# Kernel tuning notes

Measured on AMD Instinct MI355X. Metric: run time of the kernel, lower is better.

The kernel has to match this reference:

```python
import jax, jax.numpy as jnp
import numpy as np

B, L, H, V, P = 256, 16, 256, 5000, 4
NPG, DEG, STEPS, OUT = 150, 4, 4, 2000
N, E = B * NPG, B * NPG * DEG


def _seg_softmax(x, seg, num):
    # sparse softmax over variable-size groups (rows of the sparse matrix)
    m = jax.ops.segment_max(x, seg, num_segments=num)
    e = jnp.exp(x - m[seg])
    s = jax.ops.segment_sum(e, seg, num_segments=num)
    return e / s[seg]


def setup_inputs():
    key = jax.random.key(0)
    ks = jax.random.split(key, 24)
    questions = jax.random.normal(ks[0], (B, L, H), jnp.float32)
    lengths = jax.random.randint(ks[1], (B,), L // 2, L + 1)
    node_attrs = jax.random.normal(ks[2], (N, P - 1, H), jnp.float32)
    edge_attrs = jax.random.normal(ks[3], (E, H), jnp.float32)
    node_graph = jnp.repeat(jnp.arange(B), NPG)
    edge_graph = jnp.repeat(jnp.arange(B), NPG * DEG)
    off = jnp.repeat(jnp.arange(B) * NPG, NPG * DEG)
    edge_src = jax.random.randint(ks[4], (E,), 0, NPG) + off
    edge_dst = jax.random.randint(ks[5], (E,), 0, NPG) + off
    s = float(1.0 / np.sqrt(H))
    u = lambda k, shape: jax.random.uniform(k, shape, jnp.float32, -s, s)
    vocab = jax.random.normal(ks[6], (V, H), jnp.float32) * 0.1
    default_embed = jax.random.uniform(ks[7], (H,), jnp.float32)
    W_norm = jnp.eye(H, dtype=jnp.float32)
    lstm_Wih, lstm_Whh = u(ks[8], (4 * H, H)), u(ks[9], (4 * H, H))
    lstm_bih, lstm_bhh = u(ks[10], (4 * H,)), u(ks[11], (4 * H,))
    rnn_Wih, rnn_Whh = u(ks[12], (H, H)), u(ks[13], (H, H))
    rnn_bih, rnn_bhh = u(ks[14], (H,)), u(ks[15], (H,))
    prop_embeds = jax.random.normal(ks[16], (P, H), jnp.float32) * 0.1
    Ws_property = jax.random.uniform(ks[17], (P, H, H), jnp.float32) * s
    W_state = jax.random.uniform(ks[18], (H,), jnp.float32) * s
    W_relation = jax.random.uniform(ks[19], (H,), jnp.float32) * s
    lin_W, lin_b = u(ks[20], (OUT, 2 * H)), u(ks[21], (OUT,))
    return dict(questions=questions, node_attrs=node_attrs, edge_attrs=edge_attrs,
                vocab=vocab, default_embed=default_embed, W_norm=W_norm,
                lstm_Wih=lstm_Wih, lstm_Whh=lstm_Whh, lstm_bih=lstm_bih, lstm_bhh=lstm_bhh,
                rnn_Wih=rnn_Wih, rnn_Whh=rnn_Whh, rnn_bih=rnn_bih, rnn_bhh=rnn_bhh,
                prop_embeds=prop_embeds, Ws_property=Ws_property,
                W_state=W_state, W_relation=W_relation, lin_W=lin_W, lin_b=lin_b,
                lengths=lengths, node_graph=node_graph, edge_graph=edge_graph,
                edge_src=edge_src, edge_dst=edge_dst)


def reference(questions, node_attrs, edge_attrs, vocab, default_embed, W_norm,
              lstm_Wih, lstm_Whh, lstm_bih, lstm_bhh,
              rnn_Wih, rnn_Whh, rnn_bih, rnn_bhh,
              prop_embeds, Ws_property, W_state, W_relation, lin_W, lin_b,
              lengths, node_graph, edge_graph, edge_src, edge_dst):
    # ---- NormalizeWordsModel (tagger) ----
    words = questions.reshape(B * L, H)
    C = jnp.concatenate([vocab, default_embed[None]], axis=0)  # [V+1, H]
    Pm = jax.nn.softmax((words @ W_norm) @ C.T, axis=1)        # [B*L, V+1]
    Vtag = Pm[:, -1:] * words + Pm[:, :-1] @ vocab             # [B*L, H]
    Vpad = Vtag.reshape(B, L, H)

    # ---- LSTM encoder: final hidden at last valid step (packed-sequence semantics) ----
    valid = jnp.arange(L)[:, None] < lengths[None, :]  # [L, B]

    def lstm_step(carry, inp):
        h, c = carry
        x, v = inp
        g = x @ lstm_Wih.T + lstm_bih + h @ lstm_Whh.T + lstm_bhh
        i, f, gc, o = jnp.split(g, 4, axis=-1)  # torch gate order i,f,g,o
        c_new = jax.nn.sigmoid(f) * c + jax.nn.sigmoid(i) * jnp.tanh(gc)
        h_new = jax.nn.sigmoid(o) * jnp.tanh(c_new)
        vm = v[:, None]
        return (jnp.where(vm, h_new, h), jnp.where(vm, c_new, c)), None

    z = jnp.zeros((B, H), questions.dtype)
    (Q, _), _ = jax.lax.scan(lstm_step, (z, z), (Vpad.transpose(1, 0, 2), valid))

    # ---- InstructionsDecoder: relu RNNCell fed the same Q each step ----
    def dec_step(hx, _):
        hx = jax.nn.relu(Q @ rnn_Wih.T + rnn_bih + hx @ rnn_Whh.T + rnn_bhh)
        return hx, hx

    _, Hins = jax.lax.scan(dec_step, z, None, length=STEPS)
    Hins = Hins.transpose(1, 0, 2)  # [B, STEPS, H]

    # ---- attention over (masked) tagged words ----
    att = jnp.einsum('bnh,blh->bnl', Hins, Vpad)
    mask = jnp.arange(L)[None, None, :] < lengths[:, None, None]
    att = jnp.where(mask, att, -jnp.inf)
    R = jax.nn.softmax(att, axis=-1) @ Vpad  # instructions [B, STEPS, H]

    # ---- NSMCell recurrence ----
    nodes_per_graph = jax.ops.segment_sum(jnp.ones(N, questions.dtype), node_graph, num_segments=B)
    dist = (1.0 / nodes_per_graph)[node_graph]  # [N]
    prop_sim = None
    for step in range(STEPS):
        instr = R[:, step]  # [B, H]
        prop_sim = jax.nn.softmax(instr @ prop_embeds.T, axis=1)  # [B, P]
        transformed = jnp.einsum('phk,npk->nph', Ws_property[:-1], node_attrs)  # [N, P-1, H]
        node_scores = jax.nn.elu(jnp.sum(
            prop_sim[node_graph, :-1, None] * instr[node_graph, None, :] * transformed, axis=1))  # [N, H]
        edge_scores = jax.nn.elu(instr[edge_graph] * (edge_attrs @ Ws_property[-1].T))  # [E, H]
        p_state = _seg_softmax(node_scores @ W_state, node_graph, B)  # [N]
        agg = jax.ops.segment_sum(dist[edge_src, None] * edge_scores, edge_dst, num_segments=N)  # [N, H]
        p_rel = _seg_softmax(agg @ W_relation, node_graph, B)  # [N]
        r = prop_sim[node_graph, -1]
        dist = r * p_rel + (1.0 - r) * p_state

    # ---- readout ----
    node_feat = jnp.sum(prop_sim[node_graph, :-1, None] * node_attrs, axis=1)  # [N, H]
    aggregated = jax.ops.segment_sum(dist[:, None] * node_feat, node_graph, num_segments=B)  # [B, H]
    return jnp.concatenate([Q, aggregated], axis=1) @ lin_W.T + lin_b
```

## Files before the change

### kernel.cpp

```cpp
#include <hip/hip_runtime.h>
#include <hip/hip_bf16.h>
#include <math.h>

#define BB 256
#define LL 16
#define HH 256
#define VV 5000
#define NPG 150
#define DEG 4
#define NSTEPS 4
#define OUTD 2000
#define NN (BB*NPG)
#define EE (BB*NPG*DEG)
#define BL (BB*LL)
#define VPAD 5120
#define KPAD 5024

__device__ __forceinline__ float wred_sum(float v){
  #pragma unroll
  for(int o=32;o;o>>=1) v += __shfl_down(v,o,64);
  return v;
}
__device__ __forceinline__ float wred_max(float v){
  #pragma unroll
  for(int o=32;o;o>>=1) v = fmaxf(v,__shfl_down(v,o,64));
  return v;
}
__device__ __forceinline__ float block_sum256(float v, float* sh){
  v = wred_sum(v);
  __syncthreads();
  if((threadIdx.x&63)==0) sh[threadIdx.x>>6]=v;
  __syncthreads();
  return sh[0]+sh[1]+sh[2]+sh[3];
}
__device__ __forceinline__ float block_max256(float v, float* sh){
  v = wred_max(v);
  __syncthreads();
  if((threadIdx.x&63)==0) sh[threadIdx.x>>6]=v;
  __syncthreads();
  return fmaxf(fmaxf(sh[0],sh[1]),fmaxf(sh[2],sh[3]));
}
__device__ __forceinline__ float eluf(float x){ return x>0.f ? x : expm1f(x); }
__device__ __forceinline__ float sigf(float x){ return 1.f/(1.f+expf(-x)); }
__device__ __forceinline__ float fsig(float x){
  return __builtin_amdgcn_rcpf(1.f + __expf(-x));
}
__device__ __forceinline__ float ftanh(float x){
  return 1.f - 2.f*__builtin_amdgcn_rcpf(1.f + __expf(2.f*x));
}
__device__ __forceinline__ float b2f(unsigned short s){
  union{float f; unsigned int u;} x; x.u = ((unsigned int)s)<<16; return x.f;
}
__device__ __forceinline__ unsigned short f2bf_bits(float x){
  union { __hip_bfloat16 h; unsigned short s; } u; u.h = __float2bfloat16(x); return u.s;
}

__device__ __forceinline__ void async16(void* lds, const void* g){
  __builtin_amdgcn_global_load_lds(
      (const __attribute__((address_space(1))) unsigned int*)g,
      (__attribute__((address_space(3))) unsigned int*)lds, 16, 0, 0);
}

typedef __attribute__((ext_vector_type(8))) short short8;
typedef __attribute__((ext_vector_type(4))) float f32x4;

__device__ __forceinline__ short8 pack8(float4 a, float4 b){
  short8 r;
  r[0]=(short)f2bf_bits(a.x); r[1]=(short)f2bf_bits(a.y);
  r[2]=(short)f2bf_bits(a.z); r[3]=(short)f2bf_bits(a.w);
  r[4]=(short)f2bf_bits(b.x); r[5]=(short)f2bf_bits(b.y);
  r[6]=(short)f2bf_bits(b.z); r[7]=(short)f2bf_bits(b.w);
  return r;
}

template<int EPI>
__global__ __launch_bounds__(256) void mfma_bt_bf16_k(
    const __hip_bfloat16* __restrict__ A, const __hip_bfloat16* __restrict__ Bt,
    float* __restrict__ Cf, __hip_bfloat16* __restrict__ Cb,
    int lda, int ldb, int ldc, int Nreal,
    int kItersTotal, int kPerSplit, const float* __restrict__ bias,
    const float* __restrict__ rscale)
{
  __shared__ __hip_bfloat16 As[128*32];
  __shared__ __hip_bfloat16 Bs[128*32];
  const int bm = blockIdx.y*128, bn = blockIdx.x*128;
  const int tid = threadIdx.x;
  int k0 = blockIdx.z * kPerSplit;
  int k1 = k0 + kPerSplit; if (k1 > kItersTotal) k1 = kItersTotal;
  const int lane = tid & 63, wave = tid >> 6;
  const int quad = lane >> 4, r16 = lane & 15;
  const int wr = wave >> 1, wc = wave & 1;
  f32x4 acc[4][4] = {};
  const int c0 = tid, c1 = tid + 256;
  const int ar0 = c0 >> 2, ak0 = (c0 & 3)*8;
  const int ar1 = c1 >> 2, ak1 = (c1 & 3)*8;
  const __hip_bfloat16* Ab = A + (size_t)bm*lda;
  const __hip_bfloat16* Bb = Bt + (size_t)bn*ldb;
  for (int kk = k0; kk < k1; ++kk){
    const int kb = kk*32;
    async16(&As[c0*8], Ab + (size_t)ar0*lda + kb + ak0);
    async16(&As[c1*8], Ab + (size_t)ar1*lda + kb + ak1);
    async16(&Bs[c0*8], Bb + (size_t)ar0*ldb + kb + ak0);
    async16(&Bs[c1*8], Bb + (size_t)ar1*ldb + kb + ak1);
    __syncthreads();
    short8 av[4], bv[4];
    #pragma unroll
    for (int i=0;i<4;i++){
      av[i] = *(const short8*)&As[(wr*64 + i*16 + r16)*32 + quad*8];
      bv[i] = *(const short8*)&Bs[(wc*64 + i*16 + r16)*32 + quad*8];
    }
    #pragma unroll
    for (int i=0;i<4;i++)
      #pragma unroll
      for (int j=0;j<4;j++)
        acc[i][j] = __builtin_amdgcn_mfma_f32_16x16x32_bf16(av[i], bv[j], acc[i][j], 0,0,0);
    __syncthreads();
  }
  #pragma unroll
  for (int i=0;i<4;i++){
    int row = bm + wr*64 + i*16 + quad*4;
    #pragma unroll
    for (int j=0;j<4;j++){
      int col = bn + wc*64 + j*16 + r16;
      if (col >= Nreal) continue;
      #pragma unroll
      for (int r=0;r<4;r++){
        float v = acc[i][j][r];
        if (EPI==0){ if (bias) v += bias[col]; Cf[(size_t)(row+r)*ldc + col] = v; }
        else if (EPI==1){ Cb[(size_t)(row+r)*ldc + col] = __float2bfloat16(v); }
        else { if (rscale) v *= rscale[row+r]; atomicAdd(&Cf[(size_t)(row+r)*ldc + col], v); }
      }
    }
  }
}

template<int EPI>
__global__ __launch_bounds__(256) void mfma_bt_f32_k(
    const float* __restrict__ A, const float* __restrict__ Bt,
    float* __restrict__ Cf, __hip_bfloat16* __restrict__ Cb,
    int lda, int ldb, int ldc, int Nreal,
    int kIters, const float* __restrict__ bias)
{
  __shared__ __hip_bfloat16 As[128*32];
  __shared__ __hip_bfloat16 Bs[128*32];
  const int bm = blockIdx.y*128, bn = blockIdx.x*128;
  const int tid = threadIdx.x;
  const int lane = tid & 63, wave = tid >> 6;
  const int quad = lane >> 4, r16 = lane & 15;
  const int wr = wave >> 1, wc = wave & 1;
  f32x4 acc[4][4] = {};
  for (int kk = 0; kk < kIters; ++kk){
    const int kb = kk*32;
    #pragma unroll
    for (int i=0;i<2;i++){
      int c = tid + i*256;
      int row = c >> 2, k0 = (c & 3)*8;
      const float* src = A + (size_t)(bm+row)*lda + kb + k0;
      float4 v0 = *(const float4*)(src);
      float4 v1 = *(const float4*)(src+4);
      *(short8*)&As[row*32 + k0] = pack8(v0, v1);
    }
    #pragma unroll
    for (int i=0;i<2;i++){
      int c = tid + i*256;
      int row = c >> 2, k0 = (c & 3)*8;
      float4 v0 = {0.f,0.f,0.f,0.f}, v1 = {0.f,0.f,0.f,0.f};
      if (bn + row < Nreal){
        const float* src = Bt + (size_t)(bn+row)*ldb + kb + k0;
        v0 = *(const float4*)(src);
        v1 = *(const float4*)(src+4);
      }
      *(short8*)&Bs[row*32 + k0] = pack8(v0, v1);
    }
    __syncthreads();
    short8 av[4], bv[4];
    #pragma unroll
    for (int i=0;i<4;i++){
      av[i] = *(const short8*)&As[(wr*64 + i*16 + r16)*32 + quad*8];
      bv[i] = *(const short8*)&Bs[(wc*64 + i*16 + r16)*32 + quad*8];
    }
    #pragma unroll
    for (int i=0;i<4;i++)
      #pragma unroll
      for (int j=0;j<4;j++)
        acc[i][j] = __builtin_amdgcn_mfma_f32_16x16x32_bf16(av[i], bv[j], acc[i][j], 0,0,0);
    __syncthreads();
  }
  #pragma unroll
  for (int i=0;i<4;i++){
    int row = bm + wr*64 + i*16 + quad*4;
    #pragma unroll
    for (int j=0;j<4;j++){
      int col = bn + wc*64 + j*16 + r16;
      if (col >= Nreal) continue;
      #pragma unroll
      for (int r=0;r<4;r++){
        float v = acc[i][j][r];
        if (EPI==0){ if (bias) v += bias[col]; Cf[(size_t)(row+r)*ldc + col] = v; }
        else { Cb[(size_t)(row+r)*ldc + col] = __float2bfloat16(v); }
      }
    }
  }
}

__global__ __launch_bounds__(256) void gemm_exp_k(
    const __hip_bfloat16* __restrict__ A, const __hip_bfloat16* __restrict__ Bt,
    __hip_bfloat16* __restrict__ Pm, float* __restrict__ row_sum,
    float* __restrict__ e_def)
{
  __shared__ __hip_bfloat16 As[128*32];
  __shared__ __hip_bfloat16 Bs[128*32];
  const int bm = blockIdx.y*128, bn = blockIdx.x*128;
  const int tid = threadIdx.x;
  const int lane = tid & 63, wave = tid >> 6;
  const int quad = lane >> 4, r16 = lane & 15;
  const int wr = wave >> 1, wc = wave & 1;
  f32x4 acc[4][4] = {};
  const int c0 = tid, c1 = tid + 256;
  const int ar0 = c0 >> 2, ak0 = (c0 & 3)*8;
  const int ar1 = c1 >> 2, ak1 = (c1 & 3)*8;
  const __hip_bfloat16* Ab = A + (size_t)bm*HH;
  const __hip_bfloat16* Bb = Bt + (size_t)bn*HH;
  for (int kk = 0; kk < HH/32; ++kk){
    const int kb = kk*32;
    async16(&As[c0*8], Ab + (size_t)ar0*HH + kb + ak0);
    async16(&As[c1*8], Ab + (size_t)ar1*HH + kb + ak1);
    async16(&Bs[c0*8], Bb + (size_t)ar0*HH + kb + ak0);
    async16(&Bs[c1*8], Bb + (size_t)ar1*HH + kb + ak1);
    __syncthreads();
    short8 av[4], bv[4];
    #pragma unroll
    for (int i=0;i<4;i++){
      av[i] = *(const short8*)&As[(wr*64 + i*16 + r16)*32 + quad*8];
      bv[i] = *(const short8*)&Bs[(wc*64 + i*16 + r16)*32 + quad*8];
    }
    #pragma unroll
    for (int i=0;i<4;i++)
      #pragma unroll
      for (int j=0;j<4;j++)
        acc[i][j] = __builtin_amdgcn_mfma_f32_16x16x32_bf16(av[i], bv[j], acc[i][j], 0,0,0);
    __syncthreads();
  }
  #pragma unroll
  for (int i=0;i<4;i++){
    int rowb = bm + wr*64 + i*16 + quad*4;
    float rsum[4] = {0.f,0.f,0.f,0.f};
    #pragma unroll
    for (int j=0;j<4;j++){
      int col = bn + wc*64 + j*16 + r16;
      #pragma unroll
      for (int r=0;r<4;r++){
        float e = (col <= VV) ? expf(acc[i][j][r]) : 0.f;
        rsum[r] += e;
        if (col < KPAD) Pm[(size_t)(rowb+r)*KPAD + col] = __float2bfloat16(col < VV ? e : 0.f);
        if (col == VV) e_def[rowb+r] = e;
      }
    }
    #pragma unroll
    for (int r=0;r<4;r++){
      float s = rsum[r];
      s += __shfl_xor(s, 1, 64);
      s += __shfl_xor(s, 2, 64);
      s += __shfl_xor(s, 4, 64);
      s += __shfl_xor(s, 8, 64);
      if (r16 == 0) atomicAdd(&row_sum[rowb+r], s);
    }
  }
}

__global__ __launch_bounds__(1024, 4) void lstm_persist_k(
    const float* __restrict__ gX, const __hip_bfloat16* __restrict__ Whh_bf,
    const int* __restrict__ lengths,
    float* __restrict__ h_out, __hip_bfloat16* __restrict__ hbf_out)
{
  __shared__ __hip_bfloat16 Wl[512*132];
  __shared__ __hip_bfloat16 hbuf[2][16*264];
  const int bg = blockIdx.x, tid = threadIdx.x;
  const int lane = tid & 63, w = tid >> 6;
  const int quad = lane >> 4, r16 = lane & 15;
  const int hb = w*16;
  for (int idx = tid; idx < 512*16; idx += 1024){
    int row = idx >> 4, c8 = (idx & 15)*8;
    int ww = row >> 6, g = (row >> 4) & 3, rr = row & 15;
    *(short8*)&Wl[row*132 + c8] =
        *(const short8*)&Whh_bf[((size_t)(g*256 + ww*16 + rr))*256 + 128 + c8];
  }
  short8 rW[4][4];
  #pragma unroll
  for (int kc=0; kc<4; kc++)
    #pragma unroll
    for (int g=0; g<4; g++)
      rW[kc][g] = *(const short8*)&Whh_bf[((size_t)(g*256 + hb + r16))*256 + kc*32 + quad*8];
  for (int i = tid; i < 16*264; i += 1024) hbuf[0][i] = __float2bfloat16(0.f);
  int lenr[4];
  #pragma unroll
  for (int r=0;r<4;r++) lenr[r] = lengths[bg*16 + quad*4 + r];
  __syncthreads();
  f32x4 cstate = {0.f,0.f,0.f,0.f};
  f32x4 hstate = {0.f,0.f,0.f,0.f};
  int p = 0;
  const float* gXb = gX + (size_t)bg*16*LL*(4*HH) + hb + r16;
  for (int t=0; t<LL; t++){
    float gxv[4][4];
    #pragma unroll
    for (int r=0;r<4;r++)
      #pragma unroll
      for (int g=0;g<4;g++)
        gxv[r][g] = gXb[((size_t)((quad*4+r)*LL + t))*(4*HH) + g*HH];
    f32x4 acc[4] = {};
    const __hip_bfloat16* hr = hbuf[p];
    #pragma unroll
    for (int kc=0; kc<4; kc++){
      short8 a = *(const short8*)&hr[r16*264 + kc*32 + quad*8];
      #pragma unroll
      for (int g=0; g<4; g++)
        acc[g] = __builtin_amdgcn_mfma_f32_16x16x32_bf16(a, rW[kc][g], acc[g], 0,0,0);
    }
    if (w < 8){
      #pragma unroll
      for (int kc=4; kc<8; kc++){
        short8 a = *(const short8*)&hr[r16*264 + kc*32 + quad*8];
        #pragma unroll
        for (int g=0; g<4; g++){
          short8 b = *(const short8*)&Wl[(w*64 + g*16 + r16)*132 + (kc-4)*32 + quad*8];
          acc[g] = __builtin_amdgcn_mfma_f32_16x16x32_bf16(a, b, acc[g], 0,0,0);
        }
      }
    } else {
      #pragma unroll
      for (int kc=4; kc<8; kc++){
        short8 a = *(const short8*)&hr[r16*264 + kc*32 + quad*8];
        #pragma unroll
        for (int g=0; g<4; g++){
          short8 b = *(const short8*)&Whh_bf[((size_t)(g*256 + hb + r16))*256 + kc*32 + quad*8];
          acc[g] = __builtin_amdgcn_mfma_f32_16x16x32_bf16(a, b, acc[g], 0,0,0);
        }
      }
    }
    #pragma unroll
    for (int r=0;r<4;r++){
      int batch = quad*4 + r;
      float gi = acc[0][r] + gxv[r][0];
      float gf = acc[1][r] + gxv[r][1];
      float gc = acc[2][r] + gxv[r][2];
      float go = acc[3][r] + gxv[r][3];
      float cn = fsig(gf)*cstate[r] + fsig(gi)*ftanh(gc);
      float hn = fsig(go)*ftanh(cn);
      if (t < lenr[r]){ cstate[r] = cn; hstate[r] = hn; }
      hbuf[p^1][batch*264 + hb + r16] = __float2bfloat16(hstate[r]);
    }
    p ^= 1;
    __syncthreads();
  }
  #pragma unroll
  for (int r=0;r<4;r++){
    int batch = quad*4 + r;
    size_t o = (size_t)(bg*16+batch)*HH + hb + r16;
    h_out[o] = hstate[r];
    hbf_out[o] = __float2bfloat16(hstate[r]);
  }
}

__global__ __launch_bounds__(1024, 4) void dec_persist_k(
    const __hip_bfloat16* __restrict__ Qbf, const __hip_bfloat16* __restrict__ Wih_bf,
    const __hip_bfloat16* __restrict__ Whh_bf,
    const float* __restrict__ bih, const float* __restrict__ bhh,
    float* __restrict__ Hins)
{
  __shared__ __hip_bfloat16 Wl[256*264];
  __shared__ __hip_bfloat16 xb[2][16*264];
  const int bg = blockIdx.x, tid = threadIdx.x;
  const int lane = tid & 63, w = tid >> 6;
  const int quad = lane >> 4, r16 = lane & 15;
  const int col = w*16 + r16;
  for (int c = tid; c < 8192; c += 1024){
    int row = c >> 5, ci = (c & 31)*8;
    *(short8*)&Wl[row*264 + ci] = *(const short8*)&Whh_bf[(size_t)row*256 + ci];
  }
  f32x4 qp = {};
  #pragma unroll
  for (int kc=0; kc<8; kc++){
    short8 a = *(const short8*)&Qbf[(size_t)(bg*16 + r16)*HH + kc*32 + quad*8];
    short8 b = *(const short8*)&Wih_bf[(size_t)col*HH + kc*32 + quad*8];
    qp = __builtin_amdgcn_mfma_f32_16x16x32_bf16(a, b, qp, 0,0,0);
  }
  const float bihv = bih[col], bhhv = bhh[col];
  __syncthreads();
  #pragma unroll
  for (int r=0;r<4;r++){
    int batch = quad*4 + r;
    float v = fmaxf(qp[r] + bihv + bhhv, 0.f);
    xb[0][batch*264 + col] = __float2bfloat16(v);
    Hins[(size_t)(bg*16+batch)*(NSTEPS*HH) + 0*HH + col] = v;
  }
  __syncthreads();
  int p = 0;
  for (int s=1; s<NSTEPS; s++){
    f32x4 acc = {};
    #pragma unroll
    for (int kc=0; kc<8; kc++){
      short8 a = *(const short8*)&xb[p][r16*264 + kc*32 + quad*8];
      short8 b = *(const short8*)&Wl[col*264 + kc*32 + quad*8];
      acc = __builtin_amdgcn_mfma_f32_16x16x32_bf16(a, b, acc, 0,0,0);
    }
    #pragma unroll
    for (int r=0;r<4;r++){
      int batch = quad*4 + r;
      float v = fmaxf(qp[r] + bihv + acc[r] + bhhv, 0.f);
      xb[p^1][batch*264 + col] = __float2bfloat16(v);
      Hins[(size_t)(bg*16+batch)*(NSTEPS*HH) + s*HH + col] = v;
    }
    p ^= 1;
    __syncthreads();
  }
}

__global__ void cvt_bf16_k(const float* __restrict__ src, __hip_bfloat16* __restrict__ dst, int n){
  int i = (blockIdx.x*256 + threadIdx.x)*4;
  if (i >= n) return;
  float4 v = *(const float4*)(src + i);
  dst[i]   = __float2bfloat16(v.x);
  dst[i+1] = __float2bfloat16(v.y);
  dst[i+2] = __float2bfloat16(v.z);
  dst[i+3] = __float2bfloat16(v.w);
}

__global__ void tr_cvt_k(const float* __restrict__ src, __hip_bfloat16* __restrict__ dst, int R, int Ccols){
  int idx = blockIdx.x*256 + threadIdx.x;
  if (idx >= R*Ccols) return;
  int r = idx / Ccols, c = idx % Ccols;
  dst[(size_t)c*R + r] = __float2bfloat16(src[idx]);
}

__global__ void build_cb_k(const float* __restrict__ vocab, const float* __restrict__ de,
                           __hip_bfloat16* __restrict__ Cb){
  int idx = blockIdx.x*256 + threadIdx.x;
  if (idx >= VPAD*HH) return;
  int v = idx >> 8, h = idx & 255;
  float x = (v < VV) ? vocab[(size_t)v*HH + h] : (v == VV ? de[h] : 0.f);
  Cb[idx] = __float2bfloat16(x);
}

__global__ void build_vt_k(const float* __restrict__ vocab, __hip_bfloat16* __restrict__ VT){
  int idx = blockIdx.x*256 + threadIdx.x;
  if (idx >= HH*KPAD) return;
  int h = idx / KPAD, v = idx % KPAD;
  VT[idx] = __float2bfloat16(v < VV ? vocab[(size_t)v*HH + h] : 0.f);
}

__global__ void bsum_k(const float* a, const float* b, float* o){
  int i = blockIdx.x*256 + threadIdx.x;
  if (i < 4*HH) o[i] = a[i] + b[i];
}

__global__ void init_k(float* dist, float* s_rel){
  int idx = blockIdx.x*256 + threadIdx.x;
  if (idx < NN){ dist[idx] = 1.f/150.f; s_rel[idx] = 0.f; }
}

__global__ void zero_k(float* p, int n){
  int idx = blockIdx.x*256 + threadIdx.x;
  if (idx < n) p[idx] = 0.f;
}

__global__ void inv_k(float* p, int n){
  int idx = blockIdx.x*256 + threadIdx.x;
  if (idx < n) p[idx] = 1.f/p[idx];
}

__global__ void vtag_epi_k(float* __restrict__ Vtag, const float* __restrict__ e_def,
                           const float* __restrict__ inv_s, const float* __restrict__ words){
  int r = blockIdx.x, h = threadIdx.x;
  size_t o = (size_t)r*HH + h;
  Vtag[o] += e_def[r]*inv_s[r]*words[o];
}

__global__ __launch_bounds__(256) void attention_k(const float* __restrict__ Vtag,
                                                   const float* __restrict__ Hins,
                                                   const int* __restrict__ lengths,
                                                   float* __restrict__ R){
  __shared__ float Vl[LL][HH];
  __shared__ float Hn[NSTEPS][HH];
  __shared__ float att[NSTEPS][LL];
  int b = blockIdx.x, tid = threadIdx.x;
  for (int idx=tid; idx<LL*HH; idx+=256){ int l=idx>>8, h=idx&255; Vl[l][h] = Vtag[((size_t)b*LL+l)*HH + h]; }
  for (int idx=tid; idx<NSTEPS*HH; idx+=256){ Hn[idx>>8][idx&255] = Hins[(size_t)b*(NSTEPS*HH) + idx]; }
  __syncthreads();
  if (tid < NSTEPS*LL){
    int n2 = tid>>4, l = tid&15;
    float s = 0.f;
    for (int k=0;k<HH;k++) s += Hn[n2][k]*Vl[l][k];
    att[n2][l] = s;
  }
  __syncthreads();
  int len = lengths[b];
  if (tid < NSTEPS){
    float m = -1e30f;
    for (int l=0;l<len;l++) m = fmaxf(m, att[tid][l]);
    float s = 0.f;
    for (int l=0;l<LL;l++){ float e = (l<len)? expf(att[tid][l]-m) : 0.f; att[tid][l]=e; s+=e; }
    float inv = 1.f/s;
    for (int l=0;l<LL;l++) att[tid][l] *= inv;
  }
  __syncthreads();
  {
    int n2 = tid>>6, h0 = (tid&63)*4;
    float r0=0,r1=0,r2=0,r3=0;
    for (int l=0;l<LL;l++){
      float w = att[n2][l];
      r0 += w*Vl[l][h0]; r1 += w*Vl[l][h0+1]; r2 += w*Vl[l][h0+2]; r3 += w*Vl[l][h0+3];
    }
    float* o = R + (size_t)b*(NSTEPS*HH) + n2*HH + h0;
    o[0]=r0; o[1]=r1; o[2]=r2; o[3]=r3;
  }
}

__global__ __launch_bounds__(256) void prop_sim_all_k(const float* __restrict__ R,
                                                      const float* __restrict__ pe,
                                                      float* __restrict__ psa){
  __shared__ float sp[4];
  int gb = blockIdx.x;
  int s = gb >> 8, b = gb & 255;
  int tid = threadIdx.x;
  int p = tid>>6, lane = tid&63;
  const float* instr = R + (size_t)b*(NSTEPS*HH) + s*HH;
  float v = 0.f;
  for (int h=lane; h<HH; h+=64) v += instr[h]*pe[p*HH+h];
  v = wred_sum(v);
  if (lane==0) sp[p] = v;
  __syncthreads();
  if (tid==0){
    float m = fmaxf(fmaxf(sp[0],sp[1]),fmaxf(sp[2],sp[3]));
    float e0=expf(sp[0]-m), e1=expf(sp[1]-m), e2=expf(sp[2]-m), e3=expf(sp[3]-m);
    float ss = e0+e1+e2+e3;
    float* o = psa + (size_t)s*BB*4 + b*4;
    o[0]=e0/ss; o[1]=e1/ss; o[2]=e2/ss; o[3]=e3/ss;
  }
}

__global__ __launch_bounds__(256) void nsm_all_k(
    const __hip_bfloat16* __restrict__ Tf, const __hip_bfloat16* __restrict__ ET,
    const float* __restrict__ R, const float* __restrict__ psa,
    const float* __restrict__ W_state, const float* __restrict__ Wr,
    float* __restrict__ s_state_all, float* __restrict__ acc_e_all)
{
  const int wave = threadIdx.x >> 6, lane = threadIdx.x & 63;
  const int h0 = lane*4;
  if (blockIdx.x < NN/4){
    int n = blockIdx.x*4 + wave;
    int g = n / NPG;
    const unsigned short* t = (const unsigned short*)(Tf + (size_t)n*(3*HH));
    ushort4 t0 = *(const ushort4*)(t + h0);
    ushort4 t1 = *(const ushort4*)(t + HH + h0);
    ushort4 t2 = *(const ushort4*)(t + 2*HH + h0);
    float4 wv = *(const float4*)(W_state + h0);
    #pragma unroll
    for (int s=0; s<NSTEPS; s++){
      const float* instr = R + (size_t)g*(NSTEPS*HH) + s*HH;
      const float* ps = psa + (size_t)s*BB*4 + g*4;
      float ps0 = ps[0], ps1 = ps[1], ps2 = ps[2];
      float4 iv = *(const float4*)(instr + h0);
      float acc;
      acc  = eluf(iv.x*(ps0*b2f(t0.x)+ps1*b2f(t1.x)+ps2*b2f(t2.x)))*wv.x;
      acc += eluf(iv.y*(ps0*b2f(t0.y)+ps1*b2f(t1.y)+ps2*b2f(t2.y)))*wv.y;
      acc += eluf(iv.z*(ps0*b2f(t0.z)+ps1*b2f(t1.z)+ps2*b2f(t2.z)))*wv.z;
      acc += eluf(iv.w*(ps0*b2f(t0.w)+ps1*b2f(t1.w)+ps2*b2f(t2.w)))*wv.w;
      acc = wred_sum(acc);
      if (lane==0) s_state_all[(size_t)s*NN + n] = acc;
    }
  } else {
    int e = (blockIdx.x - NN/4)*4 + wave;
    int b = e / (NPG*DEG);
    const unsigned short* et = (const unsigned short*)(ET + (size_t)e*HH);
    ushort4 ev = *(const ushort4*)(et + h0);
    float4 wv = *(const float4*)(Wr + h0);
    #pragma unroll
    for (int s=0; s<NSTEPS; s++){
      const float* instr = R + (size_t)b*(NSTEPS*HH) + s*HH;
      float4 iv = *(const float4*)(instr + h0);
      float acc;
      acc  = eluf(iv.x*b2f(ev.x))*wv.x;
      acc += eluf(iv.y*b2f(ev.y))*wv.y;
      acc += eluf(iv.z*b2f(ev.z))*wv.z;
      acc += eluf(iv.w*b2f(ev.w))*wv.w;
      acc = wred_sum(acc);
      if (lane==0) acc_e_all[(size_t)s*EE + e] = acc;
    }
  }
}

__global__ void rel_scatter_k(const float* __restrict__ acc_e, const float* __restrict__ dist,
                              const int* __restrict__ esrc, const int* __restrict__ edst,
                              float* __restrict__ s_rel){
  int e = blockIdx.x*256 + threadIdx.x;
  if (e < EE) atomicAdd(&s_rel[edst[e]], dist[esrc[e]]*acc_e[e]);
}

__global__ __launch_bounds__(256) void nsm_update_k(
    const float* __restrict__ s_state, float* __restrict__ s_rel,
    const float* __restrict__ psa_s, float* __restrict__ dist)
{
  __shared__ float sh[4];
  int b = blockIdx.x, i = threadIdx.x;
  bool ok = (i < NPG);
  float ss = ok ? s_state[b*NPG + i] : -1e30f;
  float sr = ok ? s_rel[b*NPG + i]   : -1e30f;
  float m1 = block_max256(ss, sh);
  float e1 = ok ? expf(ss - m1) : 0.f;
  float d1 = block_sum256(e1, sh);
  float m2 = block_max256(sr, sh);
  float e2 = ok ? expf(sr - m2) : 0.f;
  float d2 = block_sum256(e2, sh);
  if (ok){
    float pst = e1/d1, prl = e2/d2;
    float r = psa_s[b*4+3];
    dist[b*NPG + i] = r*prl + (1.f-r)*pst;
    s_rel[b*NPG + i] = 0.f;
  }
}

__global__ __launch_bounds__(256) void final_agg_k(const float* __restrict__ na, const float* __restrict__ dist,
                                                   const float* __restrict__ ps, float* __restrict__ aggregated){
  int b = blockIdx.x, h = threadIdx.x;
  float ps0 = ps[b*4+0], ps1 = ps[b*4+1], ps2 = ps[b*4+2];
  float acc = 0.f;
  for (int i=0;i<NPG;i++){
    int n = b*NPG + i;
    float d = dist[n];
    const float* a = na + (size_t)n*(3*HH);
    acc += d*(ps0*a[h] + ps1*a[HH+h] + ps2*a[2*HH+h]);
  }
  aggregated[b*HH + h] = acc;
}

__global__ void qa_build_k(const float* __restrict__ Q, const float* __restrict__ aggregated,
                           float* __restrict__ QA){
  int idx = blockIdx.x*256 + threadIdx.x;
  if (idx >= BB*2*HH) return;
  int b = idx >> 9, k = idx & 511;
  QA[idx] = (k < HH) ? Q[b*HH + k] : aggregated[b*HH + (k-HH)];
}

extern "C" void kernel_launch(void* const* d_in, const int* in_sizes, int n_in,
                              void* d_out, int out_size, void* d_ws, size_t ws_size,
                              hipStream_t stream) {
  (void)in_sizes; (void)n_in; (void)out_size; (void)ws_size;
  const float* questions     = (const float*)d_in[0];
  const float* node_attrs    = (const float*)d_in[1];
  const float* edge_attrs    = (const float*)d_in[2];
  const float* vocab         = (const float*)d_in[3];
  const float* default_embed = (const float*)d_in[4];
  const float* W_norm        = (const float*)d_in[5];
  const float* lstm_Wih      = (const float*)d_in[6];
  const float* lstm_Whh      = (const float*)d_in[7];
  const float* lstm_bih      = (const float*)d_in[8];
  const float* lstm_bhh      = (const float*)d_in[9];
  const float* rnn_Wih       = (const float*)d_in[10];
  const float* rnn_Whh       = (const float*)d_in[11];
  const float* rnn_bih       = (const float*)d_in[12];
  const float* rnn_bhh       = (const float*)d_in[13];
  const float* prop_embeds   = (const float*)d_in[14];
  const float* Ws_property   = (const float*)d_in[15];
  const float* W_state       = (const float*)d_in[16];
  const float* W_relation    = (const float*)d_in[17];
  const float* lin_W         = (const float*)d_in[18];
  const float* lin_b         = (const float*)d_in[19];
  const int*   lengths       = (const int*)d_in[20];
  const int*   edge_src      = (const int*)d_in[23];
  const int*   edge_dst      = (const int*)d_in[24];
  float* out = (float*)d_out;

  char* base = (char*)d_ws;
  size_t off = 0;
  auto alloc = [&](size_t nbytes)->void*{
    void* p = base + off;
    off += (nbytes + 255) & ~(size_t)255;
    return p;
  };

  __hip_bfloat16* qbf     = (__hip_bfloat16*)alloc((size_t)BL*HH*2);
  __hip_bfloat16* WnT_bf  = (__hip_bfloat16*)alloc((size_t)HH*HH*2);
  __hip_bfloat16* xw_bf   = (__hip_bfloat16*)alloc((size_t)BL*HH*2);
  __hip_bfloat16* Cbv     = (__hip_bfloat16*)alloc((size_t)VPAD*HH*2);
  __hip_bfloat16* vT_bf   = (__hip_bfloat16*)alloc((size_t)HH*KPAD*2);
  __hip_bfloat16* Whh_bf  = (__hip_bfloat16*)alloc((size_t)4*HH*HH*2);
  __hip_bfloat16* rWih_bf = (__hip_bfloat16*)alloc((size_t)HH*HH*2);
  __hip_bfloat16* rWhh_bf = (__hip_bfloat16*)alloc((size_t)HH*HH*2);
  __hip_bfloat16* h_bf    = (__hip_bfloat16*)alloc((size_t)BB*HH*2);
  float* e_def    = (float*)alloc((size_t)BL*4);
  float* row_sum  = (float*)alloc((size_t)BL*4);
  float* Vtag     = (float*)alloc((size_t)BL*HH*4);
  float* bsum     = (float*)alloc((size_t)4*HH*4);
  float* h_buf    = (float*)alloc((size_t)BB*HH*4);
  float* Hins     = (float*)alloc((size_t)BB*NSTEPS*HH*4);
  float* R        = (float*)alloc((size_t)BB*NSTEPS*HH*4);
  float* psa      = (float*)alloc((size_t)NSTEPS*BB*4*4);
  float* s_state_all = (float*)alloc((size_t)NSTEPS*NN*4);
  float* acc_e_all   = (float*)alloc((size_t)NSTEPS*EE*4);
  float* s_rel    = (float*)alloc((size_t)NN*4);
  float* dist     = (float*)alloc((size_t)NN*4);
  float* aggregated = (float*)alloc((size_t)BB*HH*4);
  float* QA       = (float*)alloc((size_t)BB*2*HH*4);
  __hip_bfloat16* Pm_bf = (__hip_bfloat16*)alloc((size_t)BL*KPAD*2);
  char*  TfR      = (char*)alloc((size_t)NN*3*HH*2);
  __hip_bfloat16* Tf = (__hip_bfloat16*)TfR;
  float* gX          = (float*)TfR;
  __hip_bfloat16* ET = (__hip_bfloat16*)alloc((size_t)EE*HH*2);

  init_k<<<(NN+255)/256, 256, 0, stream>>>(dist, s_rel);
  cvt_bf16_k<<<(BL*HH/4+255)/256, 256, 0, stream>>>(questions, qbf, BL*HH);
  tr_cvt_k<<<(HH*HH+255)/256, 256, 0, stream>>>(W_norm, WnT_bf, HH, HH);
  build_cb_k<<<(VPAD*HH+255)/256, 256, 0, stream>>>(vocab, default_embed, Cbv);
  build_vt_k<<<(HH*KPAD+255)/256, 256, 0, stream>>>(vocab, vT_bf);
  cvt_bf16_k<<<(4*HH*HH/4+255)/256, 256, 0, stream>>>(lstm_Whh, Whh_bf, 4*HH*HH);
  cvt_bf16_k<<<(HH*HH/4+255)/256, 256, 0, stream>>>(rnn_Wih, rWih_bf, HH*HH);
  cvt_bf16_k<<<(HH*HH/4+255)/256, 256, 0, stream>>>(rnn_Whh, rWhh_bf, HH*HH);
  bsum_k<<<(4*HH+255)/256, 256, 0, stream>>>(lstm_bih, lstm_bhh, bsum);
  zero_k<<<(BL+255)/256, 256, 0, stream>>>(row_sum, BL);
  zero_k<<<(BL*HH+255)/256, 256, 0, stream>>>(Vtag, BL*HH);

  mfma_bt_bf16_k<1><<<dim3(2,32,1), 256, 0, stream>>>(qbf, WnT_bf, nullptr, xw_bf,
      HH, HH, HH, HH, HH/32, HH/32, nullptr, nullptr);
  gemm_exp_k<<<dim3(VPAD/128, BL/128, 1), 256, 0, stream>>>(xw_bf, Cbv, Pm_bf, row_sum, e_def);
  inv_k<<<(BL+255)/256, 256, 0, stream>>>(row_sum, BL);
  mfma_bt_bf16_k<2><<<dim3(HH/128, BL/128, 8), 256, 0, stream>>>(
      Pm_bf, vT_bf, Vtag, nullptr, KPAD, KPAD, HH, HH, KPAD/32, 20, nullptr, row_sum);
  vtag_epi_k<<<BL, HH, 0, stream>>>(Vtag, e_def, row_sum, questions);

  mfma_bt_f32_k<0><<<dim3(8,32,1), 256, 0, stream>>>(Vtag, lstm_Wih, gX, nullptr,
      HH, HH, 4*HH, 4*HH, HH/32, bsum);
  lstm_persist_k<<<16, 1024, 0, stream>>>(gX, Whh_bf, lengths, h_buf, h_bf);

  dec_persist_k<<<16, 1024, 0, stream>>>(h_bf, rWih_bf, rWhh_bf, rnn_bih, rnn_bhh, Hins);

  attention_k<<<BB, 256, 0, stream>>>(Vtag, Hins, lengths, R);
  prop_sim_all_k<<<NSTEPS*BB, 256, 0, stream>>>(R, prop_embeds, psa);

  for (int p=0; p<3; p++)
    mfma_bt_f32_k<1><<<dim3(2,NN/128,1), 256, 0, stream>>>(
        node_attrs + (size_t)p*HH, Ws_property + (size_t)p*HH*HH,
        nullptr, Tf + (size_t)p*HH, 3*HH, HH, 3*HH, HH, HH/32, nullptr);
  mfma_bt_f32_k<1><<<dim3(2,EE/128,1), 256, 0, stream>>>(
      edge_attrs, Ws_property + (size_t)3*HH*HH,
      nullptr, ET, HH, HH, HH, HH, HH/32, nullptr);

  nsm_all_k<<<NN/4 + EE/4, 256, 0, stream>>>(
      Tf, ET, R, psa, W_state, W_relation, s_state_all, acc_e_all);
  for (int s=0; s<NSTEPS; s++){
    rel_scatter_k<<<(EE+255)/256, 256, 0, stream>>>(
        acc_e_all + (size_t)s*EE, dist, edge_src, edge_dst, s_rel);
    nsm_update_k<<<BB, 256, 0, stream>>>(
        s_state_all + (size_t)s*NN, s_rel, psa + (size_t)s*BB*4, dist);
  }

  final_agg_k<<<BB, 256, 0, stream>>>(node_attrs, dist, psa + (size_t)3*BB*4, aggregated);
  qa_build_k<<<(BB*2*HH+255)/256, 256, 0, stream>>>(h_buf, aggregated, QA);
  mfma_bt_f32_k<0><<<dim3(16,2,1), 256, 0, stream>>>(QA, lin_W, out, nullptr,
      2*HH, 2*HH, OUTD, OUTD, 2*HH/32, lin_b);
}
```

Before: 1.001 ms.

## Fuse per-step relation scatter and softmax update into one per-graph kernel

Replaces the four-step loop of global-atomic scatter kernels and update kernels, plus the init kernel, with a single kernel that keeps one graph per block. Edge indices, the node distribution and the relation sums stay in shared memory, and scatter atomics go to shared memory instead of global. This removes nine kernel launches and their global round-trips. It also switches the persistent LSTM and decoder kernels from a min-blocks launch bound to an explicit waves-per-EU attribute, which may change register allocation.

```diff
diff --git a/kernel.cpp b/kernel.cpp
--- a/kernel.cpp
+++ b/kernel.cpp
@@ -15,6 +15,7 @@
 #define BL (BB*LL)
 #define VPAD 5120
 #define KPAD 5024
+#define EPG (NPG*DEG)
 
 __device__ __forceinline__ float wred_sum(float v){
   #pragma unroll
@@ -268,7 +269,9 @@
   }
 }
 
-__global__ __launch_bounds__(1024, 4) void lstm_persist_k(
+__global__ __launch_bounds__(1024)
+__attribute__((amdgpu_waves_per_eu(4, 4)))
+void lstm_persist_k(
     const float* __restrict__ gX, const __hip_bfloat16* __restrict__ Whh_bf,
     const int* __restrict__ lengths,
     float* __restrict__ h_out, __hip_bfloat16* __restrict__ hbf_out)
@@ -361,7 +364,9 @@
   }
 }
 
-__global__ __launch_bounds__(1024, 4) void dec_persist_k(
+__global__ __launch_bounds__(1024)
+__attribute__((amdgpu_waves_per_eu(4, 4)))
+void dec_persist_k(
     const __hip_bfloat16* __restrict__ Qbf, const __hip_bfloat16* __restrict__ Wih_bf,
     const __hip_bfloat16* __restrict__ Whh_bf,
     const float* __restrict__ bih, const float* __restrict__ bhh,
@@ -451,11 +456,6 @@
 __global__ void bsum_k(const float* a, const float* b, float* o){
   int i = blockIdx.x*256 + threadIdx.x;
   if (i < 4*HH) o[i] = a[i] + b[i];
-}
-
-__global__ void init_k(float* dist, float* s_rel){
-  int idx = blockIdx.x*256 + threadIdx.x;
-  if (idx < NN){ dist[idx] = 1.f/150.f; s_rel[idx] = 0.f; }
 }
 
 __global__ void zero_k(float* p, int n){
@@ -589,34 +589,47 @@
   }
 }
 
-__global__ void rel_scatter_k(const float* __restrict__ acc_e, const float* __restrict__ dist,
-                              const int* __restrict__ esrc, const int* __restrict__ edst,
-                              float* __restrict__ s_rel){
-  int e = blockIdx.x*256 + threadIdx.x;
-  if (e < EE) atomicAdd(&s_rel[edst[e]], dist[esrc[e]]*acc_e[e]);
-}
-
-__global__ __launch_bounds__(256) void nsm_update_k(
-    const float* __restrict__ s_state, float* __restrict__ s_rel,
-    const float* __restrict__ psa_s, float* __restrict__ dist)
+__global__ __launch_bounds__(256) void nsm_steps_k(
+    const float* __restrict__ s_state_all, const float* __restrict__ acc_e_all,
+    const int* __restrict__ esrc, const int* __restrict__ edst,
+    const float* __restrict__ psa, float* __restrict__ dist_out)
 {
+  __shared__ float nd[NPG];
+  __shared__ float srel[NPG];
   __shared__ float sh[4];
-  int b = blockIdx.x, i = threadIdx.x;
-  bool ok = (i < NPG);
-  float ss = ok ? s_state[b*NPG + i] : -1e30f;
-  float sr = ok ? s_rel[b*NPG + i]   : -1e30f;
-  float m1 = block_max256(ss, sh);
-  float e1 = ok ? expf(ss - m1) : 0.f;
-  float d1 = block_sum256(e1, sh);
-  float m2 = block_max256(sr, sh);
-  float e2 = ok ? expf(sr - m2) : 0.f;
-  float d2 = block_sum256(e2, sh);
-  if (ok){
-    float pst = e1/d1, prl = e2/d2;
-    float r = psa_s[b*4+3];
-    dist[b*NPG + i] = r*prl + (1.f-r)*pst;
-    s_rel[b*NPG + i] = 0.f;
-  }
+  __shared__ short les[EPG], led[EPG];
+  const int b = blockIdx.x, tid = threadIdx.x;
+  const int base_e = b*EPG, base_n = b*NPG;
+  for (int j = tid; j < EPG; j += 256){
+    les[j] = (short)(esrc[base_e + j] - base_n);
+    led[j] = (short)(edst[base_e + j] - base_n);
+  }
+  if (tid < NPG){ nd[tid] = 1.f/(float)NPG; srel[tid] = 0.f; }
+  __syncthreads();
+  for (int s=0; s<NSTEPS; s++){
+    for (int j = tid; j < EPG; j += 256){
+      float v = nd[les[j]] * acc_e_all[(size_t)s*EE + base_e + j];
+      atomicAdd(&srel[led[j]], v);
+    }
+    __syncthreads();
+    bool ok = (tid < NPG);
+    float ss = ok ? s_state_all[(size_t)s*NN + base_n + tid] : -1e30f;
+    float sr = ok ? srel[tid] : -1e30f;
+    float m1 = block_max256(ss, sh);
+    float e1 = ok ? expf(ss - m1) : 0.f;
+    float d1 = block_sum256(e1, sh);
+    float m2 = block_max256(sr, sh);
+    float e2 = ok ? expf(sr - m2) : 0.f;
+    float d2 = block_sum256(e2, sh);
+    __syncthreads();
+    if (ok){
+      float r = psa[(size_t)s*BB*4 + b*4 + 3];
+      nd[tid] = r*(e2/d2) + (1.f-r)*(e1/d1);
+      srel[tid] = 0.f;
+    }
+    __syncthreads();
+  }
+  if (tid < NPG) dist_out[base_n + tid] = nd[tid];
 }
 
 __global__ __launch_bounds__(256) void final_agg_k(const float* __restrict__ na, const float* __restrict__ dist,
@@ -697,7 +710,6 @@
   float* psa      = (float*)alloc((size_t)NSTEPS*BB*4*4);
   float* s_state_all = (float*)alloc((size_t)NSTEPS*NN*4);
   float* acc_e_all   = (float*)alloc((size_t)NSTEPS*EE*4);
-  float* s_rel    = (float*)alloc((size_t)NN*4);
   float* dist     = (float*)alloc((size_t)NN*4);
   float* aggregated = (float*)alloc((size_t)BB*HH*4);
   float* QA       = (float*)alloc((size_t)BB*2*HH*4);
@@ -707,7 +719,6 @@
   float* gX          = (float*)TfR;
   __hip_bfloat16* ET = (__hip_bfloat16*)alloc((size_t)EE*HH*2);
 
-  init_k<<<(NN+255)/256, 256, 0, stream>>>(dist, s_rel);
   cvt_bf16_k<<<(BL*HH/4+255)/256, 256, 0, stream>>>(questions, qbf, BL*HH);
   tr_cvt_k<<<(HH*HH+255)/256, 256, 0, stream>>>(W_norm, WnT_bf, HH, HH);
   build_cb_k<<<(VPAD*HH+255)/256, 256, 0, stream>>>(vocab, default_embed, Cbv);
@@ -746,12 +757,8 @@
 
   nsm_all_k<<<NN/4 + EE/4, 256, 0, stream>>>(
       Tf, ET, R, psa, W_state, W_relation, s_state_all, acc_e_all);
-  for (int s=0; s<NSTEPS; s++){
-    rel_scatter_k<<<(EE+255)/256, 256, 0, stream>>>(
-        acc_e_all + (size_t)s*EE, dist, edge_src, edge_dst, s_rel);
-    nsm_update_k<<<BB, 256, 0, stream>>>(
-        s_state_all + (size_t)s*NN, s_rel, psa + (size_t)s*BB*4, dist);
-  }
+  nsm_steps_k<<<BB, 256, 0, stream>>>(
+      s_state_all, acc_e_all, edge_src, edge_dst, psa, dist);
 
   final_agg_k<<<BB, 256, 0, stream>>>(node_attrs, dist, psa + (size_t)3*BB*4, aggregated);
   qa_build_k<<<(BB*2*HH+255)/256, 256, 0, stream>>>(h_buf, aggregated, QA);
```

After: 983.4 us. Within noise of the previous version (-1.8%).
